# Kernel optimization log

Hardware: AMD Instinct MI355X
Metric: run time of the kernel (lower is better)

The kernel has to match this reference:

```python
import jax, jax.numpy as jnp
import numpy as np

N_HEADS = 16
WINDOW = 256


def setup_inputs() -> dict:
    key = jax.random.key(0)
    ks = jax.random.split(key, 6)
    B, S, D = 2, 2048, 1024
    std = 0.02
    x = jax.random.normal(ks[0], (B, S, D), dtype=jnp.float32)
    wq = jax.random.normal(ks[1], (D, D), dtype=jnp.float32) * std
    wk = jax.random.normal(ks[2], (D, D), dtype=jnp.float32) * std
    wv = jax.random.normal(ks[3], (D, D), dtype=jnp.float32) * std
    wo = jax.random.normal(ks[4], (D, D), dtype=jnp.float32) * std
    bq = jnp.zeros((D,), jnp.float32)
    bk = jnp.zeros((D,), jnp.float32)
    bv = jnp.zeros((D,), jnp.float32)
    bo = jnp.zeros((D,), jnp.float32)
    return {"x": x, "wq": wq, "bq": bq, "wk": wk, "bk": bk,
            "wv": wv, "bv": bv, "wo": wo, "bo": bo}


def _sliding_window_bias(seq_len: int) -> jnp.ndarray:
    # allowed iff |i - j| <= WINDOW  ->  0.0, else -inf  (matches torch loop mask)
    i = jnp.arange(seq_len)[:, None]
    j = jnp.arange(seq_len)[None, :]
    allowed = jnp.abs(i - j) <= WINDOW
    return jnp.where(allowed, 0.0, -jnp.inf).astype(jnp.float32)


def reference(x, wq, bq, wk, bk, wv, bv, wo, bo):
    B, S, D = x.shape
    H = N_HEADS
    dh = D // H
    scale = dh ** -0.5
    # nn.Linear: y = x @ W^T + b
    q = (x @ wq.T + bq).reshape(B, S, H, dh).transpose(0, 2, 1, 3)  # [B,H,S,dh]
    k = (x @ wk.T + bk).reshape(B, S, H, dh).transpose(0, 2, 1, 3)
    v = (x @ wv.T + bv).reshape(B, S, H, dh).transpose(0, 2, 1, 3)
    scores = jnp.einsum('bhqd,bhkd->bhqk', q, k) * scale  # [B,H,S,S]
    scores = scores + _sliding_window_bias(S)[None, None]
    attn = jax.nn.softmax(scores, axis=-1)
    out = jnp.einsum('bhqk,bhkd->bhqd', attn, v)  # [B,H,S,dh]
    out = out.transpose(0, 2, 1, 3).reshape(B, S, D)
    return out @ wo.T + bo
```

## Files before the change

kernel.cpp:

```cpp
#include <hip/hip_runtime.h>
#include <stdint.h>

static constexpr int Ss = 2048;
static constexpr int Dd = 1024;
static constexpr int Hh = 16;
static constexpr int DH = 64;

typedef short bf16x8 __attribute__((ext_vector_type(8)));
typedef float f32x4 __attribute__((ext_vector_type(4)));

#define LOG2E 1.4426950408889634f

__device__ __forceinline__ uint16_t f2bf(float f) {
  uint32_t u = __builtin_bit_cast(uint32_t, f);
  u += 0x7fffu + ((u >> 16) & 1u);
  return (uint16_t)(u >> 16);
}
__device__ __forceinline__ float bf2f(uint16_t h) {
  uint32_t u = ((uint32_t)h) << 16;
  return __builtin_bit_cast(float, u);
}

template <int CTRL>
__device__ __forceinline__ float dppf(float x) {
  return __builtin_bit_cast(float,
      __builtin_amdgcn_update_dpp(0, __builtin_bit_cast(int, x), CTRL, 0xF, 0xF, true));
}
__device__ __forceinline__ float rowsum16(float v) {
  v += dppf<0x128>(v);
  v += dppf<0x124>(v);
  v += dppf<0x122>(v);
  v += dppf<0x121>(v);
  return v;
}
__device__ __forceinline__ float fexp2(float x) { return __builtin_amdgcn_exp2f(x); }

#define GAS(p) ((const __attribute__((address_space(1))) uint32_t*)(p))
#define LAS(p) ((__attribute__((address_space(3))) uint32_t*)(p))

__global__ void cvt_all(const float* __restrict__ x,
                        const float* __restrict__ w0, const float* __restrict__ w1,
                        const float* __restrict__ w2, const float* __restrict__ w3,
                        uint16_t* __restrict__ xb,
                        uint16_t* __restrict__ o0, uint16_t* __restrict__ o1,
                        uint16_t* __restrict__ o2, uint16_t* __restrict__ o3) {
  int bid = blockIdx.x;
  const float* in;
  uint16_t* out;
  int i;
  if (bid < 4096) {
    in = x; out = xb; i = bid * 256 + threadIdx.x;
  } else {
    int b2 = bid - 4096;
    int t = b2 >> 10;
    in = (t == 0) ? w0 : (t == 1) ? w1 : (t == 2) ? w2 : w3;
    out = (t == 0) ? o0 : (t == 1) ? o1 : (t == 2) ? o2 : o3;
    i = (b2 & 1023) * 256 + threadIdx.x;
  }
  float4 v = reinterpret_cast<const float4*>(in)[i];
  ushort4 o;
  o.x = f2bf(v.x); o.y = f2bf(v.y); o.z = f2bf(v.z); o.w = f2bf(v.w);
  reinterpret_cast<ushort4*>(out)[i] = o;
}

template <int MODE, int BN>
__global__ __launch_bounds__(256, 2) void gemm_nt(
    const uint16_t* __restrict__ A,
    const uint16_t* __restrict__ W0, const uint16_t* __restrict__ W1, const uint16_t* __restrict__ W2,
    const float* __restrict__ b0, const float* __restrict__ b1, const float* __restrict__ b2,
    void* __restrict__ O0, void* __restrict__ O1, void* __restrict__ O2,
    int M, int N, int K) {
  constexpr int NI = BN / 32;
  __shared__ __align__(16) uint8_t ldsA[128 * 128];
  __shared__ __align__(16) uint8_t ldsB[BN * 128];

  const int tid = threadIdx.x, w = tid >> 6, lane = tid & 63;
  const int q = lane & 15, g = lane >> 4;
  const int wm = w >> 1, wn = w & 1;
  const int bx = blockIdx.x, by = blockIdx.y, z = blockIdx.z;
  const uint16_t* Wp = (z == 0) ? W0 : (z == 1) ? W1 : W2;
  const float* bp = (z == 0) ? b0 : (z == 1) ? b1 : b2;
  void* Op = (z == 0) ? O0 : (z == 1) ? O1 : O2;

  f32x4 acc[4][NI] = {};

  const int nkt = K >> 6;
  for (int kt = 0; kt < nkt; ++kt) {
    const int k0 = kt << 6;
    __syncthreads();
#pragma unroll
    for (int i = 0; i < 4; ++i) {
      int Lb = w * 4096 + i * 1024 + lane * 16;
      int row = Lb >> 7, cb = Lb & 127;
      int col = (cb ^ ((row & 7) << 4)) >> 1;
      const uint16_t* srcA = A + (size_t)(bx * 128 + row) * K + k0 + col;
      __builtin_amdgcn_global_load_lds(GAS(srcA), LAS(ldsA + w * 4096 + i * 1024), 16, 0, 0);
    }
#pragma unroll
    for (int i = 0; i < BN / 32; ++i) {
      int Lb = w * (BN * 32) + i * 1024 + lane * 16;
      int row = Lb >> 7, cb = Lb & 127;
      int col = (cb ^ ((row & 7) << 4)) >> 1;
      const uint16_t* srcB = Wp + (size_t)(by * BN + row) * K + k0 + col;
      __builtin_amdgcn_global_load_lds(GAS(srcB), LAS(ldsB + w * (BN * 32) + i * 1024), 16, 0, 0);
    }
    __syncthreads();

    bf16x8 af[4][2], bfg[NI][2];
#pragma unroll
    for (int mi = 0; mi < 4; ++mi)
#pragma unroll
      for (int s = 0; s < 2; ++s) {
        int row = wm * 64 + mi * 16 + q;
        int cb = (16 * g + 64 * s) ^ ((row & 7) << 4);
        af[mi][s] = *(const bf16x8*)(ldsA + row * 128 + cb);
      }
#pragma unroll
    for (int ni = 0; ni < NI; ++ni)
#pragma unroll
      for (int s = 0; s < 2; ++s) {
        int row = wn * (BN / 2) + ni * 16 + q;
        int cb = (16 * g + 64 * s) ^ ((row & 7) << 4);
        bfg[ni][s] = *(const bf16x8*)(ldsB + row * 128 + cb);
      }
#pragma unroll
    for (int mi = 0; mi < 4; ++mi)
#pragma unroll
      for (int ni = 0; ni < NI; ++ni) {
        acc[mi][ni] = __builtin_amdgcn_mfma_f32_16x16x32_bf16(af[mi][0], bfg[ni][0], acc[mi][ni], 0, 0, 0);
        acc[mi][ni] = __builtin_amdgcn_mfma_f32_16x16x32_bf16(af[mi][1], bfg[ni][1], acc[mi][ni], 0, 0, 0);
      }
  }

  float bias[NI];
#pragma unroll
  for (int ni = 0; ni < NI; ++ni) bias[ni] = bp[by * BN + wn * (BN / 2) + ni * 16 + q];
#pragma unroll
  for (int mi = 0; mi < 4; ++mi)
#pragma unroll
    for (int ni = 0; ni < NI; ++ni)
#pragma unroll
      for (int r = 0; r < 4; ++r) {
        int m = bx * 128 + wm * 64 + mi * 16 + 4 * g + r;
        int n = by * BN + wn * (BN / 2) + ni * 16 + q;
        float v = acc[mi][ni][r] + bias[ni];
        if (MODE == 0) {
          int b = m >> 11, s = m & 2047, h = n >> 6, d = n & 63;
          ((uint16_t*)Op)[(((size_t)(b * Hh + h) * Ss + s) << 6) + d] = f2bf(v);
        } else {
          ((float*)Op)[(size_t)m * N + n] = v;
        }
      }
}

__global__ __launch_bounds__(512, 4) void attn_swa(
    const uint16_t* __restrict__ Qg, const uint16_t* __restrict__ Kg,
    const uint16_t* __restrict__ Vg, uint16_t* __restrict__ Og) {
  __shared__ __align__(16) uint8_t ldsK[2][64 * 128];
  __shared__ __align__(16) uint8_t ldsVt[2][64 * 128];
  __shared__ __align__(16) uint8_t ldsP[8][2048];

  const int tid = threadIdx.x, w = tid >> 6, lane = tid & 63;
  const int q = lane & 15, g = lane >> 4;
  const int qb = blockIdx.x, bh = blockIdx.y;
  const size_t hbase = (size_t)bh * Ss * DH;
  const uint16_t* Qp = Qg + hbase;
  const uint16_t* Kp = Kg + hbase;
  const uint16_t* Vp = Vg + hbase;
  const int q0 = qb * 128;
  const int qw = q0 + w * 16;

  bf16x8 aq[2];
#pragma unroll
  for (int s = 0; s < 2; ++s) {
    bf16x8 t = *(const bf16x8*)(Qp + (size_t)(qw + q) * DH + s * 32 + g * 8);
#pragma unroll
    for (int j = 0; j < 8; ++j) {
      float f = bf2f((uint16_t)t[j]) * 0.125f;
      t[j] = (short)f2bf(f);
    }
    aq[s] = t;
  }

  f32x4 accO[4] = {};
  float lrun[4] = {0.f, 0.f, 0.f, 0.f};

  const int t0 = (q0 >= 256) ? (q0 - 256) : 0;
  const int t1 = (q0 + 384 <= Ss) ? (q0 + 384) : Ss;
  const int nt = (t1 - t0) >> 6;

  {
    int Lb = w * 1024 + lane * 16;
    int row = Lb >> 7, cb = Lb & 127;
    const uint16_t* srcK = Kp + (size_t)(t0 + row) * DH + ((cb ^ ((row & 7) << 4)) >> 1);
    __builtin_amdgcn_global_load_lds(GAS(srcK), LAS(ldsK[0] + w * 1024), 16, 0, 0);
  }
  bf16x8 v0 = *(const bf16x8*)(Vp + (size_t)(t0 + lane) * DH + w * 8);

  for (int t = 0; t < nt; ++t) {
    const int kb0 = t0 + (t << 6);
    const int cur = t & 1, nxt = cur ^ 1;

    asm volatile("s_waitcnt vmcnt(0)" ::: "memory");
    uint8_t* Vt = ldsVt[cur];
#pragma unroll
    for (int j = 0; j < 8; ++j) {
      int c = w * 8 + j;
      *(uint16_t*)(Vt + c * 128 + ((2 * lane) ^ (j << 4))) = (uint16_t)v0[j];
    }
    asm volatile("s_waitcnt lgkmcnt(0)" ::: "memory");
    __builtin_amdgcn_sched_barrier(0);
    __builtin_amdgcn_s_barrier();
    __builtin_amdgcn_sched_barrier(0);

    if (t + 1 < nt) {
      int Lb = w * 1024 + lane * 16;
      int row = Lb >> 7, cb = Lb & 127;
      const uint16_t* srcK = Kp + (size_t)(kb0 + 64 + row) * DH + ((cb ^ ((row & 7) << 4)) >> 1);
      __builtin_amdgcn_global_load_lds(GAS(srcK), LAS(ldsK[nxt] + w * 1024), 16, 0, 0);
      v0 = *(const bf16x8*)(Vp + (size_t)(kb0 + 64 + lane) * DH + w * 8);
    }

    const int dtile = kb0 - qw;
    if (dtile >= -319 && dtile <= 271) {
      const uint8_t* Kl = ldsK[cur];
      f32x4 sacc[4] = {};
#pragma unroll
      for (int kb = 0; kb < 4; ++kb) {
        int row = kb * 16 + q;
#pragma unroll
        for (int s = 0; s < 2; ++s) {
          int cb = (16 * g + 64 * s) ^ ((row & 7) << 4);
          bf16x8 bk = *(const bf16x8*)(Kl + row * 128 + cb);
          sacc[kb] = __builtin_amdgcn_mfma_f32_16x16x32_bf16(aq[s], bk, sacc[kb], 0, 0, 0);
        }
      }
      if (dtile < -192 || dtile > 192) {
#pragma unroll
        for (int kb = 0; kb < 4; ++kb) {
          int key = kb0 + kb * 16 + q;
#pragma unroll
          for (int r = 0; r < 4; ++r) {
            int qi = qw + 4 * g + r;
            int dd = qi - key;
            bool ok = (dd <= 256) && (dd >= -256);
            sacc[kb][r] = ok ? sacc[kb][r] : -1e30f;
          }
        }
      }
      uint8_t* Pl = ldsP[w];
#pragma unroll
      for (int r = 0; r < 4; ++r) {
        float p0 = fexp2(sacc[0][r] * LOG2E);
        float p1 = fexp2(sacc[1][r] * LOG2E);
        float p2 = fexp2(sacc[2][r] * LOG2E);
        float p3 = fexp2(sacc[3][r] * LOG2E);
        float rs = rowsum16((p0 + p1) + (p2 + p3));
        lrun[r] += rs;
        int prow = 4 * g + r;
        int sw = (prow & 7) << 4;
        uint8_t* Pr = Pl + prow * 128;
        uint32_t pk01, pk23;
        asm("v_cvt_pk_bf16_f32 %0, %1, %2" : "=v"(pk01) : "v"(p0), "v"(p1));
        asm("v_cvt_pk_bf16_f32 %0, %1, %2" : "=v"(pk23) : "v"(p2), "v"(p3));
        *(uint16_t*)(Pr + ((2 * q) ^ sw))      = (uint16_t)pk01;
        *(uint16_t*)(Pr + ((2 * q + 32) ^ sw)) = (uint16_t)(pk01 >> 16);
        *(uint16_t*)(Pr + ((2 * q + 64) ^ sw)) = (uint16_t)pk23;
        *(uint16_t*)(Pr + ((2 * q + 96) ^ sw)) = (uint16_t)(pk23 >> 16);
      }
      bf16x8 ap[2];
#pragma unroll
      for (int s = 0; s < 2; ++s) {
        int cb = (16 * g + 64 * s) ^ ((q & 7) << 4);
        ap[s] = *(const bf16x8*)(Pl + q * 128 + cb);
      }
#pragma unroll
      for (int db = 0; db < 4; ++db) {
        int vr = db * 16 + q;
#pragma unroll
        for (int s = 0; s < 2; ++s) {
          int cb = (64 * s + 16 * g) ^ ((vr & 7) << 4);
          bf16x8 bvf = *(const bf16x8*)(ldsVt[cur] + vr * 128 + cb);
          accO[db] = __builtin_amdgcn_mfma_f32_16x16x32_bf16(ap[s], bvf, accO[db], 0, 0, 0);
        }
      }
    }
  }

  const int b2 = bh >> 4, h = bh & 15;
#pragma unroll
  for (int r = 0; r < 4; ++r) {
    float inv = 1.0f / lrun[r];
    int qi = qw + 4 * g + r;
    size_t rowbase = ((size_t)(b2 * Ss + qi)) * Dd + h * DH;
#pragma unroll
    for (int db = 0; db < 4; ++db) {
      Og[rowbase + db * 16 + q] = f2bf(accO[db][r] * inv);
    }
  }
}

extern "C" void kernel_launch(void* const* d_in, const int* in_sizes, int n_in,
                              void* d_out, int out_size, void* d_ws, size_t ws_size,
                              hipStream_t stream) {
  const float* x  = (const float*)d_in[0];
  const float* wq = (const float*)d_in[1];
  const float* bq = (const float*)d_in[2];
  const float* wk = (const float*)d_in[3];
  const float* bk = (const float*)d_in[4];
  const float* wv = (const float*)d_in[5];
  const float* bv = (const float*)d_in[6];
  const float* wo = (const float*)d_in[7];
  const float* bo = (const float*)d_in[8];
  float* out = (float*)d_out;

  uint8_t* ws = (uint8_t*)d_ws;
  uint16_t* xb  = (uint16_t*)(ws + (size_t)(0u  << 20));
  uint16_t* wqb = (uint16_t*)(ws + (size_t)(8u  << 20));
  uint16_t* wkb = (uint16_t*)(ws + (size_t)(10u << 20));
  uint16_t* wvb = (uint16_t*)(ws + (size_t)(12u << 20));
  uint16_t* wob = (uint16_t*)(ws + (size_t)(14u << 20));
  uint16_t* Qb  = (uint16_t*)(ws + (size_t)(16u << 20));
  uint16_t* Kb  = (uint16_t*)(ws + (size_t)(24u << 20));
  uint16_t* Vb  = (uint16_t*)(ws + (size_t)(32u << 20));
  uint16_t* AOb = (uint16_t*)(ws + (size_t)(40u << 20));

  cvt_all<<<8192, 256, 0, stream>>>(x, wq, wk, wv, wo, xb, wqb, wkb, wvb, wob);

  gemm_nt<0, 128><<<dim3(32, 8, 3), 256, 0, stream>>>(
      xb, wqb, wkb, wvb, bq, bk, bv, (void*)Qb, (void*)Kb, (void*)Vb, 4096, 1024, 1024);

  attn_swa<<<dim3(16, 32), 512, 0, stream>>>(Qb, Kb, Vb, AOb);

  gemm_nt<1, 64><<<dim3(32, 16, 1), 256, 0, stream>>>(
      AOb, wob, wob, wob, bo, bo, bo, (void*)out, (void*)out, (void*)out, 4096, 1024, 1024);
}
```

Measured before the change: 79.28 us.

## Fuse fp32-to-bf16 conversion of x into QKV GEMM with register-prefetched A tiles

Drops the separate conversion of the 16MB fp32 activation x. The QKV GEMM now loads x in fp32 straight into registers, packs it to bf16 and stores it into a double-buffered LDS tile. The next A tile is prefetched into registers while the current one is consumed, with hand-placed waitcnt and barriers. This removes a 16MB read plus 8MB write and one pass over memory, but the QKV GEMM now reads A in fp32 (twice the bytes) across all 24 N-tile blocks and carries more register pressure.

Result: slower. 81.57 us (+2.9%).

```diff
diff --git a/kernel.cpp b/kernel.cpp
--- a/kernel.cpp
+++ b/kernel.cpp
@@ -8,6 +8,7 @@
 
 typedef short bf16x8 __attribute__((ext_vector_type(8)));
 typedef float f32x4 __attribute__((ext_vector_type(4)));
+typedef uint32_t u32x4 __attribute__((ext_vector_type(4)));
 
 #define LOG2E 1.4426950408889634f
 
@@ -19,6 +20,11 @@
 __device__ __forceinline__ float bf2f(uint16_t h) {
   uint32_t u = ((uint32_t)h) << 16;
   return __builtin_bit_cast(float, u);
+}
+__device__ __forceinline__ uint32_t cvtpk(float a, float b) {
+  uint32_t r;
+  asm("v_cvt_pk_bf16_f32 %0, %1, %2" : "=v"(r) : "v"(a), "v"(b));
+  return r;
 }
 
 template <int CTRL>
@@ -38,41 +44,29 @@
 #define GAS(p) ((const __attribute__((address_space(1))) uint32_t*)(p))
 #define LAS(p) ((__attribute__((address_space(3))) uint32_t*)(p))
 
-__global__ void cvt_all(const float* __restrict__ x,
-                        const float* __restrict__ w0, const float* __restrict__ w1,
-                        const float* __restrict__ w2, const float* __restrict__ w3,
-                        uint16_t* __restrict__ xb,
-                        uint16_t* __restrict__ o0, uint16_t* __restrict__ o1,
-                        uint16_t* __restrict__ o2, uint16_t* __restrict__ o3) {
+__global__ void cvt_w(const float* __restrict__ w0, const float* __restrict__ w1,
+                      const float* __restrict__ w2, const float* __restrict__ w3,
+                      uint16_t* __restrict__ o0, uint16_t* __restrict__ o1,
+                      uint16_t* __restrict__ o2, uint16_t* __restrict__ o3) {
   int bid = blockIdx.x;
-  const float* in;
-  uint16_t* out;
-  int i;
-  if (bid < 4096) {
-    in = x; out = xb; i = bid * 256 + threadIdx.x;
-  } else {
-    int b2 = bid - 4096;
-    int t = b2 >> 10;
-    in = (t == 0) ? w0 : (t == 1) ? w1 : (t == 2) ? w2 : w3;
-    out = (t == 0) ? o0 : (t == 1) ? o1 : (t == 2) ? o2 : o3;
-    i = (b2 & 1023) * 256 + threadIdx.x;
-  }
+  int t = bid >> 10;
+  const float* in = (t == 0) ? w0 : (t == 1) ? w1 : (t == 2) ? w2 : w3;
+  uint16_t* out = (t == 0) ? o0 : (t == 1) ? o1 : (t == 2) ? o2 : o3;
+  int i = (bid & 1023) * 256 + threadIdx.x;
   float4 v = reinterpret_cast<const float4*>(in)[i];
   ushort4 o;
   o.x = f2bf(v.x); o.y = f2bf(v.y); o.z = f2bf(v.z); o.w = f2bf(v.w);
   reinterpret_cast<ushort4*>(out)[i] = o;
 }
 
-template <int MODE, int BN>
-__global__ __launch_bounds__(256, 2) void gemm_nt(
-    const uint16_t* __restrict__ A,
+__global__ __launch_bounds__(256, 2) void gemm_qkv(
+    const float* __restrict__ X,
     const uint16_t* __restrict__ W0, const uint16_t* __restrict__ W1, const uint16_t* __restrict__ W2,
     const float* __restrict__ b0, const float* __restrict__ b1, const float* __restrict__ b2,
-    void* __restrict__ O0, void* __restrict__ O1, void* __restrict__ O2,
-    int M, int N, int K) {
-  constexpr int NI = BN / 32;
-  __shared__ __align__(16) uint8_t ldsA[128 * 128];
-  __shared__ __align__(16) uint8_t ldsB[BN * 128];
+    uint16_t* __restrict__ O0, uint16_t* __restrict__ O1, uint16_t* __restrict__ O2) {
+  constexpr int K = 1024;
+  __shared__ __align__(16) uint8_t ldsA[2][128 * 128];
+  __shared__ __align__(16) uint8_t ldsB[128 * 128];
 
   const int tid = threadIdx.x, w = tid >> 6, lane = tid & 63;
   const int q = lane & 15, g = lane >> 4;
@@ -80,9 +74,123 @@
   const int bx = blockIdx.x, by = blockIdx.y, z = blockIdx.z;
   const uint16_t* Wp = (z == 0) ? W0 : (z == 1) ? W1 : W2;
   const float* bp = (z == 0) ? b0 : (z == 1) ? b1 : b2;
-  void* Op = (z == 0) ? O0 : (z == 1) ? O1 : O2;
-
-  f32x4 acc[4][NI] = {};
+  uint16_t* Op = (z == 0) ? O0 : (z == 1) ? O1 : O2;
+
+  int arow[4], aelem[4];
+#pragma unroll
+  for (int i = 0; i < 4; ++i) {
+    int Lb = w * 4096 + i * 1024 + lane * 16;
+    int row = Lb >> 7, cb = Lb & 127;
+    arow[i] = row;
+    aelem[i] = (cb ^ ((row & 7) << 4)) >> 1;
+  }
+
+  f32x4 acc[4][4] = {};
+  float4 ar[4][2];
+
+#pragma unroll
+  for (int i = 0; i < 4; ++i) {
+    const float* s = X + (size_t)(bx * 128 + arow[i]) * K + aelem[i];
+    ar[i][0] = *(const float4*)s;
+    ar[i][1] = *(const float4*)(s + 4);
+  }
+
+  const int nkt = K >> 6;
+  for (int kt = 0; kt < nkt; ++kt) {
+    const int k0 = kt << 6;
+    const int cur = kt & 1;
+
+    __builtin_amdgcn_s_barrier();
+    __builtin_amdgcn_sched_barrier(0);
+#pragma unroll
+    for (int i = 0; i < 4; ++i) {
+      int Lb = w * 4096 + i * 1024 + lane * 16;
+      int row = Lb >> 7, cb = Lb & 127;
+      const uint16_t* srcB = Wp + (size_t)(by * 128 + row) * K + k0 + ((cb ^ ((row & 7) << 4)) >> 1);
+      __builtin_amdgcn_global_load_lds(GAS(srcB), LAS(ldsB + w * 4096 + i * 1024), 16, 0, 0);
+    }
+    __builtin_amdgcn_sched_barrier(0);
+#pragma unroll
+    for (int i = 0; i < 4; ++i) {
+      u32x4 pk;
+      pk[0] = cvtpk(ar[i][0].x, ar[i][0].y);
+      pk[1] = cvtpk(ar[i][0].z, ar[i][0].w);
+      pk[2] = cvtpk(ar[i][1].x, ar[i][1].y);
+      pk[3] = cvtpk(ar[i][1].z, ar[i][1].w);
+      *(u32x4*)(ldsA[cur] + w * 4096 + i * 1024 + lane * 16) = pk;
+    }
+    __builtin_amdgcn_sched_barrier(0);
+    if (kt + 1 < nkt) {
+#pragma unroll
+      for (int i = 0; i < 4; ++i) {
+        const float* s = X + (size_t)(bx * 128 + arow[i]) * K + (k0 + 64) + aelem[i];
+        ar[i][0] = *(const float4*)s;
+        ar[i][1] = *(const float4*)(s + 4);
+      }
+      __builtin_amdgcn_sched_barrier(0);
+      asm volatile("s_waitcnt vmcnt(8) lgkmcnt(0)" ::: "memory");
+    } else {
+      asm volatile("s_waitcnt vmcnt(0) lgkmcnt(0)" ::: "memory");
+    }
+    __builtin_amdgcn_sched_barrier(0);
+    __builtin_amdgcn_s_barrier();
+    __builtin_amdgcn_sched_barrier(0);
+
+    bf16x8 af[4][2], bfg[4][2];
+#pragma unroll
+    for (int mi = 0; mi < 4; ++mi)
+#pragma unroll
+      for (int s = 0; s < 2; ++s) {
+        int row = wm * 64 + mi * 16 + q;
+        int cb = (16 * g + 64 * s) ^ ((row & 7) << 4);
+        af[mi][s] = *(const bf16x8*)(ldsA[cur] + row * 128 + cb);
+      }
+#pragma unroll
+    for (int ni = 0; ni < 4; ++ni)
+#pragma unroll
+      for (int s = 0; s < 2; ++s) {
+        int row = wn * 64 + ni * 16 + q;
+        int cb = (16 * g + 64 * s) ^ ((row & 7) << 4);
+        bfg[ni][s] = *(const bf16x8*)(ldsB + row * 128 + cb);
+      }
+#pragma unroll
+    for (int mi = 0; mi < 4; ++mi)
+#pragma unroll
+      for (int ni = 0; ni < 4; ++ni) {
+        acc[mi][ni] = __builtin_amdgcn_mfma_f32_16x16x32_bf16(af[mi][0], bfg[ni][0], acc[mi][ni], 0, 0, 0);
+        acc[mi][ni] = __builtin_amdgcn_mfma_f32_16x16x32_bf16(af[mi][1], bfg[ni][1], acc[mi][ni], 0, 0, 0);
+      }
+  }
+
+  float bias[4];
+#pragma unroll
+  for (int ni = 0; ni < 4; ++ni) bias[ni] = bp[by * 128 + wn * 64 + ni * 16 + q];
+#pragma unroll
+  for (int mi = 0; mi < 4; ++mi)
+#pragma unroll
+    for (int ni = 0; ni < 4; ++ni)
+#pragma unroll
+      for (int r = 0; r < 4; ++r) {
+        int m = bx * 128 + wm * 64 + mi * 16 + 4 * g + r;
+        int n = by * 128 + wn * 64 + ni * 16 + q;
+        float v = acc[mi][ni][r] + bias[ni];
+        int b = m >> 11, s = m & 2047, h = n >> 6, d = n & 63;
+        Op[(((size_t)(b * Hh + h) * Ss + s) << 6) + d] = f2bf(v);
+      }
+}
+
+__global__ __launch_bounds__(256, 2) void gemm_out(
+    const uint16_t* __restrict__ A, const uint16_t* __restrict__ W,
+    const float* __restrict__ bp, float* __restrict__ O, int M, int N, int K) {
+  __shared__ __align__(16) uint8_t ldsA[128 * 128];
+  __shared__ __align__(16) uint8_t ldsB[64 * 128];
+
+  const int tid = threadIdx.x, w = tid >> 6, lane = tid & 63;
+  const int q = lane & 15, g = lane >> 4;
+  const int wm = w >> 1, wn = w & 1;
+  const int bx = blockIdx.x, by = blockIdx.y;
+
+  f32x4 acc[4][2] = {};
 
   const int nkt = K >> 6;
   for (int kt = 0; kt < nkt; ++kt) {
@@ -92,21 +200,19 @@
     for (int i = 0; i < 4; ++i) {
       int Lb = w * 4096 + i * 1024 + lane * 16;
       int row = Lb >> 7, cb = Lb & 127;
-      int col = (cb ^ ((row & 7) << 4)) >> 1;
-      const uint16_t* srcA = A + (size_t)(bx * 128 + row) * K + k0 + col;
+      const uint16_t* srcA = A + (size_t)(bx * 128 + row) * K + k0 + ((cb ^ ((row & 7) << 4)) >> 1);
       __builtin_amdgcn_global_load_lds(GAS(srcA), LAS(ldsA + w * 4096 + i * 1024), 16, 0, 0);
     }
 #pragma unroll
-    for (int i = 0; i < BN / 32; ++i) {
-      int Lb = w * (BN * 32) + i * 1024 + lane * 16;
+    for (int i = 0; i < 2; ++i) {
+      int Lb = w * 2048 + i * 1024 + lane * 16;
       int row = Lb >> 7, cb = Lb & 127;
-      int col = (cb ^ ((row & 7) << 4)) >> 1;
-      const uint16_t* srcB = Wp + (size_t)(by * BN + row) * K + k0 + col;
-      __builtin_amdgcn_global_load_lds(GAS(srcB), LAS(ldsB + w * (BN * 32) + i * 1024), 16, 0, 0);
+      const uint16_t* srcB = W + (size_t)(by * 64 + row) * K + k0 + ((cb ^ ((row & 7) << 4)) >> 1);
+      __builtin_amdgcn_global_load_lds(GAS(srcB), LAS(ldsB + w * 2048 + i * 1024), 16, 0, 0);
     }
     __syncthreads();
 
-    bf16x8 af[4][2], bfg[NI][2];
+    bf16x8 af[4][2], bfg[2][2];
 #pragma unroll
     for (int mi = 0; mi < 4; ++mi)
 #pragma unroll
@@ -116,40 +222,34 @@
         af[mi][s] = *(const bf16x8*)(ldsA + row * 128 + cb);
       }
 #pragma unroll
-    for (int ni = 0; ni < NI; ++ni)
+    for (int ni = 0; ni < 2; ++ni)
 #pragma unroll
       for (int s = 0; s < 2; ++s) {
-        int row = wn * (BN / 2) + ni * 16 + q;
+        int row = wn * 32 + ni * 16 + q;
         int cb = (16 * g + 64 * s) ^ ((row & 7) << 4);
         bfg[ni][s] = *(const bf16x8*)(ldsB + row * 128 + cb);
       }
 #pragma unroll
     for (int mi = 0; mi < 4; ++mi)
 #pragma unroll
-      for (int ni = 0; ni < NI; ++ni) {
+      for (int ni = 0; ni < 2; ++ni) {
         acc[mi][ni] = __builtin_amdgcn_mfma_f32_16x16x32_bf16(af[mi][0], bfg[ni][0], acc[mi][ni], 0, 0, 0);
         acc[mi][ni] = __builtin_amdgcn_mfma_f32_16x16x32_bf16(af[mi][1], bfg[ni][1], acc[mi][ni], 0, 0, 0);
       }
   }
 
-  float bias[NI];
-#pragma unroll
-  for (int ni = 0; ni < NI; ++ni) bias[ni] = bp[by * BN + wn * (BN / 2) + ni * 16 + q];
+  float bias[2];
+#pragma unroll
+  for (int ni = 0; ni < 2; ++ni) bias[ni] = bp[by * 64 + wn * 32 + ni * 16 + q];
 #pragma unroll
   for (int mi = 0; mi < 4; ++mi)
 #pragma unroll
-    for (int ni = 0; ni < NI; ++ni)
+    for (int ni = 0; ni < 2; ++ni)
 #pragma unroll
       for (int r = 0; r < 4; ++r) {
         int m = bx * 128 + wm * 64 + mi * 16 + 4 * g + r;
-        int n = by * BN + wn * (BN / 2) + ni * 16 + q;
-        float v = acc[mi][ni][r] + bias[ni];
-        if (MODE == 0) {
-          int b = m >> 11, s = m & 2047, h = n >> 6, d = n & 63;
-          ((uint16_t*)Op)[(((size_t)(b * Hh + h) * Ss + s) << 6) + d] = f2bf(v);
-        } else {
-          ((float*)Op)[(size_t)m * N + n] = v;
-        }
+        int n = by * 64 + wn * 32 + ni * 16 + q;
+        O[(size_t)m * N + n] = acc[mi][ni][r] + bias[ni];
       }
 }
 
@@ -260,9 +360,7 @@
         int prow = 4 * g + r;
         int sw = (prow & 7) << 4;
         uint8_t* Pr = Pl + prow * 128;
-        uint32_t pk01, pk23;
-        asm("v_cvt_pk_bf16_f32 %0, %1, %2" : "=v"(pk01) : "v"(p0), "v"(p1));
-        asm("v_cvt_pk_bf16_f32 %0, %1, %2" : "=v"(pk23) : "v"(p2), "v"(p3));
+        uint32_t pk01 = cvtpk(p0, p1), pk23 = cvtpk(p2, p3);
         *(uint16_t*)(Pr + ((2 * q) ^ sw))      = (uint16_t)pk01;
         *(uint16_t*)(Pr + ((2 * q + 32) ^ sw)) = (uint16_t)(pk01 >> 16);
         *(uint16_t*)(Pr + ((2 * q + 64) ^ sw)) = (uint16_t)pk23;
@@ -315,23 +413,22 @@
   float* out = (float*)d_out;
 
   uint8_t* ws = (uint8_t*)d_ws;
-  uint16_t* xb  = (uint16_t*)(ws + (size_t)(0u  << 20));
-  uint16_t* wqb = (uint16_t*)(ws + (size_t)(8u  << 20));
-  uint16_t* wkb = (uint16_t*)(ws + (size_t)(10u << 20));
-  uint16_t* wvb = (uint16_t*)(ws + (size_t)(12u << 20));
-  uint16_t* wob = (uint16_t*)(ws + (size_t)(14u << 20));
-  uint16_t* Qb  = (uint16_t*)(ws + (size_t)(16u << 20));
-  uint16_t* Kb  = (uint16_t*)(ws + (size_t)(24u << 20));
-  uint16_t* Vb  = (uint16_t*)(ws + (size_t)(32u << 20));
-  uint16_t* AOb = (uint16_t*)(ws + (size_t)(40u << 20));
-
-  cvt_all<<<8192, 256, 0, stream>>>(x, wq, wk, wv, wo, xb, wqb, wkb, wvb, wob);
-
-  gemm_nt<0, 128><<<dim3(32, 8, 3), 256, 0, stream>>>(
-      xb, wqb, wkb, wvb, bq, bk, bv, (void*)Qb, (void*)Kb, (void*)Vb, 4096, 1024, 1024);
+  uint16_t* wqb = (uint16_t*)(ws + (size_t)(0u  << 20));
+  uint16_t* wkb = (uint16_t*)(ws + (size_t)(2u  << 20));
+  uint16_t* wvb = (uint16_t*)(ws + (size_t)(4u  << 20));
+  uint16_t* wob = (uint16_t*)(ws + (size_t)(6u  << 20));
+  uint16_t* Qb  = (uint16_t*)(ws + (size_t)(8u  << 20));
+  uint16_t* Kb  = (uint16_t*)(ws + (size_t)(16u << 20));
+  uint16_t* Vb  = (uint16_t*)(ws + (size_t)(24u << 20));
+  uint16_t* AOb = (uint16_t*)(ws + (size_t)(32u << 20));
+
+  cvt_w<<<4096, 256, 0, stream>>>(wq, wk, wv, wo, wqb, wkb, wvb, wob);
+
+  gemm_qkv<<<dim3(32, 8, 3), 256, 0, stream>>>(
+      x, wqb, wkb, wvb, bq, bk, bv, Qb, Kb, Vb);
 
   attn_swa<<<dim3(16, 32), 512, 0, stream>>>(Qb, Kb, Vb, AOb);
 
-  gemm_nt<1, 64><<<dim3(32, 16, 1), 256, 0, stream>>>(
-      AOb, wob, wob, wob, bo, bo, bo, (void*)out, (void*)out, (void*)out, 4096, 1024, 1024);
-}
+  gemm_out<<<dim3(32, 16), 256, 0, stream>>>(
+      AOb, wob, bo, out, 4096, 1024, 1024);
+}
```
